# Kernel optimization log

Hardware: AMD Instinct MI355X
Metric: run time of the kernel (lower is better)

## Reference

```python
import jax, jax.numpy as jnp
import numpy as np

B, C, H, W = 8, 256, 64, 64
CQK = C // 8  # 32


def setup_inputs() -> dict:
    key = jax.random.key(0)
    ks = jax.random.split(key, 7)
    s = 0.02
    return {
        "feat_map": jax.random.normal(ks[0], (B, C, H, W), dtype=jnp.float32),
        "w1": jax.random.normal(ks[1], (CQK, C), dtype=jnp.float32) * s,
        "b1": jnp.zeros((CQK,), dtype=jnp.float32),
        "w2": jax.random.normal(ks[2], (CQK, C), dtype=jnp.float32) * s,
        "b2": jnp.zeros((CQK,), dtype=jnp.float32),
        "w3": jax.random.normal(ks[3], (C, C), dtype=jnp.float32) * s,
        "b3": jnp.zeros((C,), dtype=jnp.float32),
        "gamma": jnp.zeros((1,), dtype=jnp.float32),
    }


def reference(feat_map, w1, b1, w2, b2, w3, b3, gamma):
    b, c, h, w = feat_map.shape
    n = h * w
    x = feat_map.reshape(b, c, n)  # [B, C, N]
    # 1x1 convs == per-pixel linear maps over channels
    q = jnp.einsum("oc,bcn->bno", w1, x) + b1  # [B, N, C//8]
    k = jnp.einsum("oc,bcn->bon", w2, x) + b2[None, :, None]  # [B, C//8, N]
    v = jnp.einsum("oc,bcn->bon", w3, x) + b3[None, :, None]  # [B, C, N]
    relation = jnp.einsum("bno,bom->bnm", q, k)  # [B, N, N]
    attn = jax.nn.softmax(relation, axis=-1)  # softmax over last dim
    # feat_refine = bmm(v, attn^T): out[:, :, i] = sum_j v[:, :, j] * attn[i, j]
    feat_refine = jnp.einsum("bcm,bnm->bcn", v, attn).reshape(b, c, h, w)
    scaled = gamma[0] * feat_refine
    return (feat_refine, scaled)
```

## Files before the change

kernel.cpp:

```cpp
#include <hip/hip_runtime.h>
#include <cmath>

#define NB 8
#define CC 256
#define NPIX 4096
#define QB 64
#define KVB 64
#define NT (NPIX / KVB)
#define LOG2E 1.4426950408889634f

typedef __attribute__((ext_vector_type(4))) float f32x4;
typedef __attribute__((ext_vector_type(8))) short s16x8;
typedef __attribute__((ext_vector_type(4))) unsigned short u16x4;
typedef __attribute__((ext_vector_type(4))) unsigned int u32x4;
typedef __attribute__((ext_vector_type(2))) unsigned int u32x2;

__device__ __forceinline__ unsigned short f2bf(float f) {
    union { float f; unsigned int u; } v; v.f = f;
    return (unsigned short)((v.u + 0x7FFFu + ((v.u >> 16) & 1u)) >> 16);
}

__device__ __forceinline__ unsigned int cvt_pk_bf16(float lo, float hi) {
    unsigned int r;
    asm("v_cvt_pk_bf16_f32 %0, %1, %2" : "=v"(r) : "v"(lo), "v"(hi));
    return r;
}

__device__ __forceinline__ float u2f(unsigned int u) {
    union { unsigned int u; float f; } v; v.u = u; return v.f;
}

__global__ __launch_bounds__(320) void proj_gemm_kernel(
    const float* __restrict__ x,
    const float* __restrict__ w1, const float* __restrict__ b1,
    const float* __restrict__ w2, const float* __restrict__ b2,
    const float* __restrict__ w3, const float* __restrict__ b3,
    unsigned short* __restrict__ Qm, unsigned short* __restrict__ Km,
    unsigned short* __restrict__ Vm)
{
    const int b  = blockIdx.x >> 6;
    const int n0 = (blockIdx.x & 63) * 64;
    const int wave = threadIdx.x >> 6;
    const int lane = threadIdx.x & 63;
    const int cl = lane & 15, g = lane >> 4;

    const float* arow[4];
#pragma unroll
    for (int ct = 0; ct < 4; ++ct) {
        const int row = wave * 64 + ct * 16 + cl;
        if (row < 32)       arow[ct] = w1 + (size_t)row * 256;
        else if (row < 64)  arow[ct] = w2 + (size_t)(row - 32) * 256;
        else                arow[ct] = w3 + (size_t)(row - 64) * 256;
    }

    const float* xb = x + (size_t)b * CC * NPIX + n0 + cl;

    f32x4 acc[4][4];
#pragma unroll
    for (int ct = 0; ct < 4; ++ct)
#pragma unroll
        for (int nt = 0; nt < 4; ++nt) acc[ct][nt] = (f32x4){0.f, 0.f, 0.f, 0.f};

    for (int ks = 0; ks < 8; ++ks) {
        const int c0 = ks * 32;
        s16x8 ah[4];
#pragma unroll
        for (int ct = 0; ct < 4; ++ct) {
            const float* ap = arow[ct] + c0 + g * 8;
            f32x4 a0 = *(const f32x4*)ap;
            f32x4 a1 = *(const f32x4*)(ap + 4);
            u32x4 u;
            u[0] = cvt_pk_bf16(a0[0], a0[1]); u[1] = cvt_pk_bf16(a0[2], a0[3]);
            u[2] = cvt_pk_bf16(a1[0], a1[1]); u[3] = cvt_pk_bf16(a1[2], a1[3]);
            ah[ct] = __builtin_bit_cast(s16x8, u);
        }
#pragma unroll
        for (int nt = 0; nt < 4; ++nt) {
            const float* xp = xb + (size_t)(c0 + g * 8) * NPIX + nt * 16;
            float xe[8];
#pragma unroll
            for (int e = 0; e < 8; ++e) xe[e] = xp[(size_t)e * NPIX];
            u32x4 uh, ul;
#pragma unroll
            for (int p = 0; p < 4; ++p) {
                const unsigned int hp = cvt_pk_bf16(xe[2 * p], xe[2 * p + 1]);
                const float h0 = u2f(hp << 16);
                const float h1 = u2f(hp & 0xffff0000u);
                uh[p] = hp;
                ul[p] = cvt_pk_bf16(xe[2 * p] - h0, xe[2 * p + 1] - h1);
            }
            const s16x8 bh = __builtin_bit_cast(s16x8, uh);
            const s16x8 bl = __builtin_bit_cast(s16x8, ul);
#pragma unroll
            for (int ct = 0; ct < 4; ++ct)
                acc[ct][nt] = __builtin_amdgcn_mfma_f32_16x16x32_bf16(ah[ct], bh, acc[ct][nt], 0, 0, 0);
#pragma unroll
            for (int ct = 0; ct < 4; ++ct)
                acc[ct][nt] = __builtin_amdgcn_mfma_f32_16x16x32_bf16(ah[ct], bl, acc[ct][nt], 0, 0, 0);
        }
    }

    if (wave == 0) {
#pragma unroll
        for (int ct = 0; ct < 4; ++ct) {
#pragma unroll
            for (int nt = 0; nt < 4; ++nt) {
                const int n = n0 + nt * 16 + cl;
                const int co = ct * 16 + g * 4;
                f32x4 v = acc[ct][nt];
                if (ct < 2) {
                    const float q0 = (v[0] + b1[co + 0]) * LOG2E;
                    const float q1 = (v[1] + b1[co + 1]) * LOG2E;
                    const float q2 = (v[2] + b1[co + 2]) * LOG2E;
                    const float q3 = (v[3] + b1[co + 3]) * LOG2E;
                    u32x2 dd = {cvt_pk_bf16(q0, q1), cvt_pk_bf16(q2, q3)};
                    *(u32x2*)(Qm + ((size_t)b * NPIX + n) * 32 + co) = dd;
                } else {
                    const int ko = co - 32;
                    const float k0 = v[0] + b2[ko + 0];
                    const float k1 = v[1] + b2[ko + 1];
                    const float k2 = v[2] + b2[ko + 2];
                    const float k3 = v[3] + b2[ko + 3];
                    u32x2 dd = {cvt_pk_bf16(k0, k1), cvt_pk_bf16(k2, k3)};
                    *(u32x2*)(Km + ((size_t)b * NPIX + n) * 32 + ko) = dd;
                }
            }
        }
    } else {
        const int cvb = (wave - 1) * 64;
#pragma unroll
        for (int ct = 0; ct < 4; ++ct) {
#pragma unroll
            for (int nt = 0; nt < 4; ++nt) {
                const int n = n0 + nt * 16 + cl;
                const int cv = cvb + ct * 16 + g * 4;
#pragma unroll
                for (int r = 0; r < 4; ++r)
                    Vm[((size_t)b * CC + cv + r) * NPIX + n] = f2bf(acc[ct][nt][r] + b3[cv + r]);
            }
        }
    }
}

__global__ __launch_bounds__(512, 4) void attn_kernel(
    const unsigned short* __restrict__ Qm, const unsigned short* __restrict__ Km,
    const unsigned short* __restrict__ Vm, const float* __restrict__ gamma,
    float* __restrict__ out)
{
    __shared__ unsigned short Vs[CC * KVB];
    __shared__ unsigned short Ps[QB * KVB];
    __shared__ float alpha_lds[QB];
    __shared__ float l_lds[QB];

    const int bid = ((blockIdx.x & 7) << 6) + (blockIdx.x >> 3);
    const int b = bid >> 6;
    const int q0 = (bid & 63) * QB;

    const int t = threadIdx.x;
    const int wave = t >> 6;
    const int lane = t & 63;
    const int cl = lane & 15;
    const int g = lane >> 4;
    const int c0w = wave * 32;
    const bool owner = wave < 4;
    const int qrow_own = (wave & 3) * 16 + cl;

    const s16x8 qf = *(const s16x8*)(Qm + (((size_t)b * NPIX) + q0 + qrow_own) * 32 + g * 8);

    f32x4 acc[4][2];
#pragma unroll
    for (int qt = 0; qt < 4; ++qt)
#pragma unroll
        for (int ct = 0; ct < 2; ++ct)
            acc[qt][ct] = (f32x4){0.f, 0.f, 0.f, 0.f};

    float mrun = -__builtin_inff();
    float lrun = 0.f;

    const unsigned short* Kg = Km + (size_t)b * NPIX * 32;
    const unsigned short* Vg = Vm + (size_t)b * CC * NPIX;

    const int vin = t & 7;
    const int vr0 = t >> 3;
    const unsigned short* vsrc = Vg + (size_t)vr0 * NPIX + vin * 8;
    unsigned short* vdst = &Vs[vr0 * 64 + ((vin ^ (vr0 & 7)) << 3)];

    s16x8 vreg[4];
#pragma unroll
    for (int i = 0; i < 4; ++i)
        vreg[i] = *(const s16x8*)(vsrc + (size_t)i * 64 * NPIX);

    s16x8 kf[4];
#pragma unroll
    for (int mt = 0; mt < 4; ++mt)
        kf[mt] = *(const s16x8*)(Kg + (size_t)(mt * 16 + cl) * 32 + g * 8);

    for (int it = 0; it < NT; ++it) {
        __syncthreads();

#pragma unroll
        for (int i = 0; i < 4; ++i)
            *(s16x8*)(vdst + i * 64 * 64) = vreg[i];

        {
            const int mn = ((it + 1) & (NT - 1)) * KVB;
#pragma unroll
            for (int i = 0; i < 4; ++i)
                vreg[i] = *(const s16x8*)(vsrc + (size_t)i * 64 * NPIX + mn);
        }

        if (owner) {
            f32x4 s[4];
            __builtin_amdgcn_s_setprio(1);
#pragma unroll
            for (int mt = 0; mt < 4; ++mt) {
                f32x4 z = (f32x4){0.f, 0.f, 0.f, 0.f};
                s[mt] = __builtin_amdgcn_mfma_f32_16x16x32_bf16(kf[mt], qf, z, 0, 0, 0);
            }
            __builtin_amdgcn_s_setprio(0);

            float ml = -__builtin_inff();
#pragma unroll
            for (int mt = 0; mt < 4; ++mt)
#pragma unroll
                for (int r = 0; r < 4; ++r) ml = fmaxf(ml, s[mt][r]);
            ml = fmaxf(ml, __shfl_xor(ml, 16, 64));
            ml = fmaxf(ml, __shfl_xor(ml, 32, 64));

            float alpha = 1.f;
            if (!__all(ml <= mrun + 8.f)) {
                const float mnew = fmaxf(mrun, ml);
                alpha = __builtin_amdgcn_exp2f(mrun - mnew);
                mrun = mnew;
                lrun *= alpha;
            }
            if (g == 0) alpha_lds[qrow_own] = alpha;

#pragma unroll
            for (int mt = 0; mt < 4; ++mt) {
#pragma unroll
                for (int r = 0; r < 4; ++r) {
                    s[mt][r] = __builtin_amdgcn_exp2f(s[mt][r] - mrun);
                    lrun += s[mt][r];
                }
            }

#pragma unroll
            for (int mt = 0; mt < 4; ++mt) {
                u32x2 dd = {cvt_pk_bf16(s[mt][0], s[mt][1]),
                            cvt_pk_bf16(s[mt][2], s[mt][3])};
                *(u32x2*)(&Ps[qrow_own * 64 + ((mt * 16 + g * 4) ^ ((qrow_own & 7) << 3))]) = dd;
            }

            const int mnext = ((it + 1) & (NT - 1)) * KVB;
#pragma unroll
            for (int mt = 0; mt < 4; ++mt)
                kf[mt] = *(const s16x8*)(Kg + (size_t)(mnext + mt * 16 + cl) * 32 + g * 8);
        }

        __syncthreads();

        float aq[4];
#pragma unroll
        for (int qt = 0; qt < 4; ++qt) aq[qt] = alpha_lds[qt * 16 + cl];
        if (__any(aq[0] != 1.f || aq[1] != 1.f || aq[2] != 1.f || aq[3] != 1.f)) {
#pragma unroll
            for (int qt = 0; qt < 4; ++qt)
#pragma unroll
                for (int ct = 0; ct < 2; ++ct) acc[qt][ct] *= aq[qt];
        }

#pragma unroll
        for (int ch = 0; ch < 2; ++ch) {
            s16x8 pb[4];
#pragma unroll
            for (int qt = 0; qt < 4; ++qt) {
                const int qr = qt * 16 + cl;
                pb[qt] = *(const s16x8*)(&Ps[qr * 64 + ((ch * 32 + g * 8) ^ ((qr & 7) << 3))]);
            }
            __builtin_amdgcn_s_setprio(1);
#pragma unroll
            for (int ct = 0; ct < 2; ++ct) {
                const int cr = c0w + ct * 16 + cl;
                s16x8 av = *(const s16x8*)(&Vs[cr * 64 + ((ch * 32 + g * 8) ^ ((cr & 7) << 3))]);
#pragma unroll
                for (int qt = 0; qt < 4; ++qt)
                    acc[qt][ct] = __builtin_amdgcn_mfma_f32_16x16x32_bf16(av, pb[qt], acc[qt][ct], 0, 0, 0);
            }
            __builtin_amdgcn_s_setprio(0);
        }
    }

    if (owner) {
        lrun += __shfl_xor(lrun, 16, 64);
        lrun += __shfl_xor(lrun, 32, 64);
        if (g == 0) l_lds[qrow_own] = lrun;
    }
    __syncthreads();

    const float gm = gamma[0];
    float* out2 = out + (size_t)NB * CC * NPIX;
#pragma unroll
    for (int qt = 0; qt < 4; ++qt) {
        const float inv = 1.f / l_lds[qt * 16 + cl];
        const int n = q0 + qt * 16 + cl;
#pragma unroll
        for (int ct = 0; ct < 2; ++ct) {
#pragma unroll
            for (int r = 0; r < 4; ++r) {
                const int chn = c0w + ct * 16 + g * 4 + r;
                const float val = acc[qt][ct][r] * inv;
                const size_t idx = ((size_t)b * CC + chn) * NPIX + n;
                out[idx] = val;
                out2[idx] = gm * val;
            }
        }
    }
}

extern "C" void kernel_launch(void* const* d_in, const int* in_sizes, int n_in,
                              void* d_out, int out_size, void* d_ws, size_t ws_size,
                              hipStream_t stream) {
    (void)in_sizes; (void)n_in; (void)out_size; (void)ws_size;
    const float* x     = (const float*)d_in[0];
    const float* w1    = (const float*)d_in[1];
    const float* b1    = (const float*)d_in[2];
    const float* w2    = (const float*)d_in[3];
    const float* b2    = (const float*)d_in[4];
    const float* w3    = (const float*)d_in[5];
    const float* b3    = (const float*)d_in[6];
    const float* gamma = (const float*)d_in[7];
    float* out = (float*)d_out;

    unsigned short* Qm = (unsigned short*)d_ws;
    unsigned short* Km = Qm + (size_t)NB * NPIX * 32;
    unsigned short* Vm = Km + (size_t)NB * NPIX * 32;

    proj_gemm_kernel<<<NB * 64, 320, 0, stream>>>(x, w1, b1, w2, b2, w3, b3, Qm, Km, Vm);
    attn_kernel<<<NB * 64, 512, 0, stream>>>(Qm, Km, Vm, gamma, out);
}
```

Baseline: 143.4 us.

## Software-pipeline softmax one tile ahead and rebalance PV channels across waves

Double-buffers the P tile and alpha scale in LDS so the owner waves compute QK^T/softmax for tile it+1 while all waves run the PV MFMAs for tile it. A prologue handles tile 0 before the loop. It also gives owner waves 16 channels and the other waves 48 each, to offset the softmax work the owners carry. This adds a second barrier per iteration, more LDS, and a 3-wide accumulator with runtime-guarded tiles, which may raise register pressure and add divergence.

```diff
diff --git a/kernel.cpp b/kernel.cpp
--- a/kernel.cpp
+++ b/kernel.cpp
@@ -148,8 +148,8 @@
     float* __restrict__ out)
 {
     __shared__ unsigned short Vs[CC * KVB];
-    __shared__ unsigned short Ps[QB * KVB];
-    __shared__ float alpha_lds[QB];
+    __shared__ unsigned short Ps[2][QB * KVB];
+    __shared__ float alpha_lds[2][QB];
     __shared__ float l_lds[QB];
 
     const int bid = ((blockIdx.x & 7) << 6) + (blockIdx.x >> 3);
@@ -161,17 +161,18 @@
     const int lane = t & 63;
     const int cl = lane & 15;
     const int g = lane >> 4;
-    const int c0w = wave * 32;
     const bool owner = wave < 4;
+    const int c0w = owner ? (wave * 16) : (64 + (wave - 4) * 48);
+    const int NCT = owner ? 1 : 3;
     const int qrow_own = (wave & 3) * 16 + cl;
 
     const s16x8 qf = *(const s16x8*)(Qm + (((size_t)b * NPIX) + q0 + qrow_own) * 32 + g * 8);
 
-    f32x4 acc[4][2];
+    f32x4 acc[4][3];
 #pragma unroll
     for (int qt = 0; qt < 4; ++qt)
 #pragma unroll
-        for (int ct = 0; ct < 2; ++ct)
+        for (int ct = 0; ct < 3; ++ct)
             acc[qt][ct] = (f32x4){0.f, 0.f, 0.f, 0.f};
 
     float mrun = -__builtin_inff();
@@ -191,17 +192,53 @@
         vreg[i] = *(const s16x8*)(vsrc + (size_t)i * 64 * NPIX);
 
     s16x8 kf[4];
-#pragma unroll
-    for (int mt = 0; mt < 4; ++mt)
-        kf[mt] = *(const s16x8*)(Kg + (size_t)(mt * 16 + cl) * 32 + g * 8);
+    if (owner) {
+#pragma unroll
+        for (int mt = 0; mt < 4; ++mt)
+            kf[mt] = *(const s16x8*)(Kg + (size_t)(mt * 16 + cl) * 32 + g * 8);
+
+        f32x4 s[4];
+#pragma unroll
+        for (int mt = 0; mt < 4; ++mt) {
+            f32x4 z = (f32x4){0.f, 0.f, 0.f, 0.f};
+            s[mt] = __builtin_amdgcn_mfma_f32_16x16x32_bf16(kf[mt], qf, z, 0, 0, 0);
+        }
+        float ml = -__builtin_inff();
+#pragma unroll
+        for (int mt = 0; mt < 4; ++mt)
+#pragma unroll
+            for (int r = 0; r < 4; ++r) ml = fmaxf(ml, s[mt][r]);
+        ml = fmaxf(ml, __shfl_xor(ml, 16, 64));
+        ml = fmaxf(ml, __shfl_xor(ml, 32, 64));
+        mrun = ml;
+        if (g == 0) alpha_lds[0][qrow_own] = 1.f;
+#pragma unroll
+        for (int mt = 0; mt < 4; ++mt) {
+#pragma unroll
+            for (int r = 0; r < 4; ++r) {
+                s[mt][r] = __builtin_amdgcn_exp2f(s[mt][r] - mrun);
+                lrun += s[mt][r];
+            }
+        }
+#pragma unroll
+        for (int mt = 0; mt < 4; ++mt) {
+            u32x2 dd = {cvt_pk_bf16(s[mt][0], s[mt][1]),
+                        cvt_pk_bf16(s[mt][2], s[mt][3])};
+            *(u32x2*)(&Ps[0][qrow_own * 64 + ((mt * 16 + g * 4) ^ ((qrow_own & 7) << 3))]) = dd;
+        }
+#pragma unroll
+        for (int mt = 0; mt < 4; ++mt)
+            kf[mt] = *(const s16x8*)(Kg + (size_t)(KVB + mt * 16 + cl) * 32 + g * 8);
+    }
 
     for (int it = 0; it < NT; ++it) {
+        const int buf = it & 1;
+
         __syncthreads();
 
 #pragma unroll
         for (int i = 0; i < 4; ++i)
             *(s16x8*)(vdst + i * 64 * 64) = vreg[i];
-
         {
             const int mn = ((it + 1) & (NT - 1)) * KVB;
 #pragma unroll
@@ -209,7 +246,19 @@
                 vreg[i] = *(const s16x8*)(vsrc + (size_t)i * 64 * NPIX + mn);
         }
 
-        if (owner) {
+        __syncthreads();
+
+        float aq[4];
+#pragma unroll
+        for (int qt = 0; qt < 4; ++qt) aq[qt] = alpha_lds[buf][qt * 16 + cl];
+        if (__any(aq[0] != 1.f || aq[1] != 1.f || aq[2] != 1.f || aq[3] != 1.f)) {
+#pragma unroll
+            for (int qt = 0; qt < 4; ++qt)
+#pragma unroll
+                for (int ct = 0; ct < 3; ++ct) acc[qt][ct] *= aq[qt];
+        }
+
+        if (owner && it < NT - 1) {
             f32x4 s[4];
             __builtin_amdgcn_s_setprio(1);
 #pragma unroll
@@ -234,7 +283,7 @@
                 mrun = mnew;
                 lrun *= alpha;
             }
-            if (g == 0) alpha_lds[qrow_own] = alpha;
+            if (g == 0) alpha_lds[buf ^ 1][qrow_own] = alpha;
 
 #pragma unroll
             for (int mt = 0; mt < 4; ++mt) {
@@ -244,48 +293,37 @@
                     lrun += s[mt][r];
                 }
             }
-
 #pragma unroll
             for (int mt = 0; mt < 4; ++mt) {
                 u32x2 dd = {cvt_pk_bf16(s[mt][0], s[mt][1]),
                             cvt_pk_bf16(s[mt][2], s[mt][3])};
-                *(u32x2*)(&Ps[qrow_own * 64 + ((mt * 16 + g * 4) ^ ((qrow_own & 7) << 3))]) = dd;
-            }
-
-            const int mnext = ((it + 1) & (NT - 1)) * KVB;
+                *(u32x2*)(&Ps[buf ^ 1][qrow_own * 64 + ((mt * 16 + g * 4) ^ ((qrow_own & 7) << 3))]) = dd;
+            }
+
+            const int mnext = ((it + 2) & (NT - 1)) * KVB;
 #pragma unroll
             for (int mt = 0; mt < 4; ++mt)
                 kf[mt] = *(const s16x8*)(Kg + (size_t)(mnext + mt * 16 + cl) * 32 + g * 8);
         }
 
-        __syncthreads();
-
-        float aq[4];
-#pragma unroll
-        for (int qt = 0; qt < 4; ++qt) aq[qt] = alpha_lds[qt * 16 + cl];
-        if (__any(aq[0] != 1.f || aq[1] != 1.f || aq[2] != 1.f || aq[3] != 1.f)) {
-#pragma unroll
-            for (int qt = 0; qt < 4; ++qt)
-#pragma unroll
-                for (int ct = 0; ct < 2; ++ct) acc[qt][ct] *= aq[qt];
-        }
-
 #pragma unroll
         for (int ch = 0; ch < 2; ++ch) {
             s16x8 pb[4];
 #pragma unroll
             for (int qt = 0; qt < 4; ++qt) {
                 const int qr = qt * 16 + cl;
-                pb[qt] = *(const s16x8*)(&Ps[qr * 64 + ((ch * 32 + g * 8) ^ ((qr & 7) << 3))]);
+                pb[qt] = *(const s16x8*)(&Ps[buf][qr * 64 + ((ch * 32 + g * 8) ^ ((qr & 7) << 3))]);
             }
             __builtin_amdgcn_s_setprio(1);
 #pragma unroll
-            for (int ct = 0; ct < 2; ++ct) {
-                const int cr = c0w + ct * 16 + cl;
-                s16x8 av = *(const s16x8*)(&Vs[cr * 64 + ((ch * 32 + g * 8) ^ ((cr & 7) << 3))]);
-#pragma unroll
-                for (int qt = 0; qt < 4; ++qt)
-                    acc[qt][ct] = __builtin_amdgcn_mfma_f32_16x16x32_bf16(av, pb[qt], acc[qt][ct], 0, 0, 0);
+            for (int ct = 0; ct < 3; ++ct) {
+                if (ct < NCT) {
+                    const int cr = c0w + ct * 16 + cl;
+                    s16x8 av = *(const s16x8*)(&Vs[cr * 64 + ((ch * 32 + g * 8) ^ ((cr & 7) << 3))]);
+#pragma unroll
+                    for (int qt = 0; qt < 4; ++qt)
+                        acc[qt][ct] = __builtin_amdgcn_mfma_f32_16x16x32_bf16(av, pb[qt], acc[qt][ct], 0, 0, 0);
+                }
             }
             __builtin_amdgcn_s_setprio(0);
         }
@@ -305,14 +343,16 @@
         const float inv = 1.f / l_lds[qt * 16 + cl];
         const int n = q0 + qt * 16 + cl;
 #pragma unroll
-        for (int ct = 0; ct < 2; ++ct) {
-#pragma unroll
-            for (int r = 0; r < 4; ++r) {
-                const int chn = c0w + ct * 16 + g * 4 + r;
-                const float val = acc[qt][ct][r] * inv;
-                const size_t idx = ((size_t)b * CC + chn) * NPIX + n;
-                out[idx] = val;
-                out2[idx] = gm * val;
+        for (int ct = 0; ct < 3; ++ct) {
+            if (ct < NCT) {
+#pragma unroll
+                for (int r = 0; r < 4; ++r) {
+                    const int chn = c0w + ct * 16 + g * 4 + r;
+                    const float val = acc[qt][ct][r] * inv;
+                    const size_t idx = ((size_t)b * CC + chn) * NPIX + n;
+                    out[idx] = val;
+                    out2[idx] = gm * val;
+                }
             }
         }
     }
```

Result: slower. 149.6 us (+4.3%).

## Tile V by key block and load MFMA operands directly from global memory

Applied to the files above, without the earlier changes.

The projection kernel now writes V in a blocked layout [b][key tile][channel][64], so each key tile's V slab is contiguous. The attention kernel drops the V shared-memory staging and loads its MFMA A operands straight from global memory (mostly L2). Channel work is rebalanced so the softmax-owner waves take 16 channels and the other waves take 48. The cross-lane max shuffles now run only when a rescale is needed. This removes LDS traffic and barrier pressure for V, but exposes global load latency inside the loop because there is no prefetch, and it adds more accumulator registers.

```diff
diff --git a/kernel.cpp b/kernel.cpp
--- a/kernel.cpp
+++ b/kernel.cpp
@@ -36,7 +36,7 @@
     const float* __restrict__ w2, const float* __restrict__ b2,
     const float* __restrict__ w3, const float* __restrict__ b3,
     unsigned short* __restrict__ Qm, unsigned short* __restrict__ Km,
-    unsigned short* __restrict__ Vm)
+    unsigned short* __restrict__ Vt)
 {
     const int b  = blockIdx.x >> 6;
     const int n0 = (blockIdx.x & 63) * 64;
@@ -128,15 +128,17 @@
         }
     } else {
         const int cvb = (wave - 1) * 64;
+        const int mt0 = n0 >> 6;
 #pragma unroll
         for (int ct = 0; ct < 4; ++ct) {
 #pragma unroll
             for (int nt = 0; nt < 4; ++nt) {
-                const int n = n0 + nt * 16 + cl;
+                const int ni = nt * 16 + cl;
                 const int cv = cvb + ct * 16 + g * 4;
 #pragma unroll
                 for (int r = 0; r < 4; ++r)
-                    Vm[((size_t)b * CC + cv + r) * NPIX + n] = f2bf(acc[ct][nt][r] + b3[cv + r]);
+                    Vt[((size_t)(b * 64 + mt0) * CC + cv + r) * 64 + ni] =
+                        f2bf(acc[ct][nt][r] + b3[cv + r]);
             }
         }
     }
@@ -144,10 +146,9 @@
 
 __global__ __launch_bounds__(512, 4) void attn_kernel(
     const unsigned short* __restrict__ Qm, const unsigned short* __restrict__ Km,
-    const unsigned short* __restrict__ Vm, const float* __restrict__ gamma,
+    const unsigned short* __restrict__ Vt, const float* __restrict__ gamma,
     float* __restrict__ out)
 {
-    __shared__ unsigned short Vs[CC * KVB];
     __shared__ unsigned short Ps[QB * KVB];
     __shared__ float alpha_lds[QB];
     __shared__ float l_lds[QB];
@@ -161,52 +162,45 @@
     const int lane = t & 63;
     const int cl = lane & 15;
     const int g = lane >> 4;
-    const int c0w = wave * 32;
     const bool owner = wave < 4;
+    const int c0w = owner ? (wave * 16) : (64 + (wave - 4) * 48);
+    const int NCT = owner ? 1 : 3;
     const int qrow_own = (wave & 3) * 16 + cl;
 
     const s16x8 qf = *(const s16x8*)(Qm + (((size_t)b * NPIX) + q0 + qrow_own) * 32 + g * 8);
 
-    f32x4 acc[4][2];
+    f32x4 acc[4][3];
 #pragma unroll
     for (int qt = 0; qt < 4; ++qt)
 #pragma unroll
-        for (int ct = 0; ct < 2; ++ct)
+        for (int ct = 0; ct < 3; ++ct)
             acc[qt][ct] = (f32x4){0.f, 0.f, 0.f, 0.f};
 
     float mrun = -__builtin_inff();
     float lrun = 0.f;
 
     const unsigned short* Kg = Km + (size_t)b * NPIX * 32;
-    const unsigned short* Vg = Vm + (size_t)b * CC * NPIX;
-
-    const int vin = t & 7;
-    const int vr0 = t >> 3;
-    const unsigned short* vsrc = Vg + (size_t)vr0 * NPIX + vin * 8;
-    unsigned short* vdst = &Vs[vr0 * 64 + ((vin ^ (vr0 & 7)) << 3)];
-
-    s16x8 vreg[4];
-#pragma unroll
-    for (int i = 0; i < 4; ++i)
-        vreg[i] = *(const s16x8*)(vsrc + (size_t)i * 64 * NPIX);
+    const unsigned short* vbase = Vt + ((size_t)b * 64 * CC + c0w + cl) * 64 + g * 8;
 
     s16x8 kf[4];
-#pragma unroll
-    for (int mt = 0; mt < 4; ++mt)
-        kf[mt] = *(const s16x8*)(Kg + (size_t)(mt * 16 + cl) * 32 + g * 8);
+    if (owner) {
+#pragma unroll
+        for (int mt = 0; mt < 4; ++mt)
+            kf[mt] = *(const s16x8*)(Kg + (size_t)(mt * 16 + cl) * 32 + g * 8);
+    }
 
     for (int it = 0; it < NT; ++it) {
         __syncthreads();
 
-#pragma unroll
-        for (int i = 0; i < 4; ++i)
-            *(s16x8*)(vdst + i * 64 * 64) = vreg[i];
-
+        s16x8 av[2][3];
         {
-            const int mn = ((it + 1) & (NT - 1)) * KVB;
-#pragma unroll
-            for (int i = 0; i < 4; ++i)
-                vreg[i] = *(const s16x8*)(vsrc + (size_t)i * 64 * NPIX + mn);
+            const unsigned short* vit = vbase + (size_t)it * CC * 64;
+#pragma unroll
+            for (int ch = 0; ch < 2; ++ch)
+#pragma unroll
+                for (int ct = 0; ct < 3; ++ct)
+                    if (ct < NCT)
+                        av[ch][ct] = *(const s16x8*)(vit + (size_t)(ct * 16) * 64 + ch * 32);
         }
 
         if (owner) {
@@ -224,11 +218,11 @@
             for (int mt = 0; mt < 4; ++mt)
 #pragma unroll
                 for (int r = 0; r < 4; ++r) ml = fmaxf(ml, s[mt][r]);
-            ml = fmaxf(ml, __shfl_xor(ml, 16, 64));
-            ml = fmaxf(ml, __shfl_xor(ml, 32, 64));
 
             float alpha = 1.f;
             if (!__all(ml <= mrun + 8.f)) {
+                ml = fmaxf(ml, __shfl_xor(ml, 16, 64));
+                ml = fmaxf(ml, __shfl_xor(ml, 32, 64));
                 const float mnew = fmaxf(mrun, ml);
                 alpha = __builtin_amdgcn_exp2f(mrun - mnew);
                 mrun = mnew;
@@ -267,7 +261,7 @@
 #pragma unroll
             for (int qt = 0; qt < 4; ++qt)
 #pragma unroll
-                for (int ct = 0; ct < 2; ++ct) acc[qt][ct] *= aq[qt];
+                for (int ct = 0; ct < 3; ++ct) acc[qt][ct] *= aq[qt];
         }
 
 #pragma unroll
@@ -280,12 +274,12 @@
             }
             __builtin_amdgcn_s_setprio(1);
 #pragma unroll
-            for (int ct = 0; ct < 2; ++ct) {
-                const int cr = c0w + ct * 16 + cl;
-                s16x8 av = *(const s16x8*)(&Vs[cr * 64 + ((ch * 32 + g * 8) ^ ((cr & 7) << 3))]);
-#pragma unroll
-                for (int qt = 0; qt < 4; ++qt)
-                    acc[qt][ct] = __builtin_amdgcn_mfma_f32_16x16x32_bf16(av, pb[qt], acc[qt][ct], 0, 0, 0);
+            for (int ct = 0; ct < 3; ++ct) {
+                if (ct < NCT) {
+#pragma unroll
+                    for (int qt = 0; qt < 4; ++qt)
+                        acc[qt][ct] = __builtin_amdgcn_mfma_f32_16x16x32_bf16(av[ch][ct], pb[qt], acc[qt][ct], 0, 0, 0);
+                }
             }
             __builtin_amdgcn_s_setprio(0);
         }
@@ -305,14 +299,16 @@
         const float inv = 1.f / l_lds[qt * 16 + cl];
         const int n = q0 + qt * 16 + cl;
 #pragma unroll
-        for (int ct = 0; ct < 2; ++ct) {
-#pragma unroll
-            for (int r = 0; r < 4; ++r) {
-                const int chn = c0w + ct * 16 + g * 4 + r;
-                const float val = acc[qt][ct][r] * inv;
-                const size_t idx = ((size_t)b * CC + chn) * NPIX + n;
-                out[idx] = val;
-                out2[idx] = gm * val;
+        for (int ct = 0; ct < 3; ++ct) {
+            if (ct < NCT) {
+#pragma unroll
+                for (int r = 0; r < 4; ++r) {
+                    const int chn = c0w + ct * 16 + g * 4 + r;
+                    const float val = acc[qt][ct][r] * inv;
+                    const size_t idx = ((size_t)b * CC + chn) * NPIX + n;
+                    out[idx] = val;
+                    out2[idx] = gm * val;
+                }
             }
         }
     }
@@ -334,8 +330,8 @@
 
     unsigned short* Qm = (unsigned short*)d_ws;
     unsigned short* Km = Qm + (size_t)NB * NPIX * 32;
-    unsigned short* Vm = Km + (size_t)NB * NPIX * 32;
-
-    proj_gemm_kernel<<<NB * 64, 320, 0, stream>>>(x, w1, b1, w2, b2, w3, b3, Qm, Km, Vm);
-    attn_kernel<<<NB * 64, 512, 0, stream>>>(Qm, Km, Vm, gamma, out);
-}
+    unsigned short* Vt = Km + (size_t)NB * NPIX * 32;
+
+    proj_gemm_kernel<<<NB * 64, 320, 0, stream>>>(x, w1, b1, w2, b2, w3, b3, Qm, Km, Vt);
+    attn_kernel<<<NB * 64, 512, 0, stream>>>(Qm, Km, Vt, gamma, out);
+}
```

Measured after the change: 193.5 us. 1.35x slower.
